# Kernel optimization log

Hardware: AMD Instinct MI355X
Metric: run time of the kernel (lower is better)

Reference implementation:

```python
import jax, jax.numpy as jnp
import numpy as np

B, T, C, H = 4, 2048, 768, 12
D = C // H  # head dim = 64


def setup_inputs() -> dict:
    key = jax.random.key(0)
    ks = jax.random.split(key, 4)
    scale = 0.02
    return {
        "x": jax.random.normal(ks[0], (B, T, C), dtype=jnp.float32),
        "W_attn": jax.random.normal(ks[1], (C, 3 * C), dtype=jnp.float32) * scale,
        "b_attn": jnp.zeros((3 * C,), dtype=jnp.float32),
        "W_proj": jax.random.normal(ks[2], (C, C), dtype=jnp.float32) * scale,
        "b_proj": jnp.zeros((C,), dtype=jnp.float32),
    }


def reference(x, W_attn, b_attn, W_proj, b_proj):
    Bsz, Tlen, Cdim = x.shape
    qkv = x @ W_attn + b_attn                    # [B,T,3C]
    q, k, v = jnp.split(qkv, 3, axis=-1)          # each [B,T,C]
    # [B,T,C] -> [B,H,T,D]
    def heads(t):
        return t.reshape(Bsz, Tlen, H, D).transpose(0, 2, 1, 3)
    q, k, v = heads(q), heads(k), heads(v)
    att = jnp.einsum("bhqd,bhkd->bhqk", q, k) * (1.0 / np.sqrt(D))
    # causal mask: position q attends to k <= q
    mask = jnp.tril(jnp.ones((Tlen, Tlen), dtype=bool))
    att = jnp.where(mask[None, None], att, -jnp.inf)
    att = jax.nn.softmax(att, axis=-1)
    y = jnp.einsum("bhqk,bhkd->bhqd", att, v)     # [B,H,T,D]
    y = y.transpose(0, 2, 1, 3).reshape(Bsz, Tlen, Cdim)
    return y @ W_proj + b_proj
```

## Files before the change

kernel.cpp:

```cpp
#include <hip/hip_runtime.h>

#define B_SZ   4
#define T_LEN  2048
#define C_DIM  768
#define H_NUM  12
#define THREEC (3 * C_DIM)
#define M_ROWS (B_SZ * T_LEN)
#define CAST_N8 (M_ROWS * C_DIM / 8)
#define CAST_BLOCKS (CAST_N8 / 256)
#define TP_BX ((THREEC + C_DIM) / 32)
#define TP_BY (C_DIM / 32)

typedef _Float16 f16;
typedef _Float16 half8 __attribute__((ext_vector_type(8)));
typedef _Float16 half4 __attribute__((ext_vector_type(4)));
typedef __fp16   pk2   __attribute__((ext_vector_type(2)));
typedef float    f32x4 __attribute__((ext_vector_type(4)));

#define GLD16(gaddr, laddr)                                                         \
  __builtin_amdgcn_global_load_lds(                                                 \
      (const __attribute__((address_space(1))) unsigned int*)(gaddr),               \
      (__attribute__((address_space(3))) unsigned int*)(laddr), 16, 0, 0)
#define MFMA16(a, b, c) __builtin_amdgcn_mfma_f32_16x16x32_f16(a, b, c, 0, 0, 0)

__global__ __launch_bounds__(256) void prep_kernel(
    const float* __restrict__ x, f16* __restrict__ xh,
    const float* __restrict__ Wa, const float* __restrict__ Wp,
    f16* __restrict__ WtA, f16* __restrict__ WtP) {
  __shared__ f16 tile[32][33];
  const int bid = blockIdx.x;
  if (bid < CAST_BLOCKS) {
    int i = bid * 256 + threadIdx.x;
    const float* s = x + (size_t)i * 8;
    half8 h;
#pragma unroll
    for (int u = 0; u < 8; ++u) h[u] = (f16)s[u];
    *(half8*)(xh + (size_t)i * 8) = h;
    return;
  }
  const int t = bid - CAST_BLOCKS;
  int bx = t % TP_BX;
  const int by = t / TP_BX;
  const float* W; f16* Wt; int N;
  if (bx < THREEC / 32) { W = Wa; Wt = WtA; N = THREEC; }
  else { W = Wp; Wt = WtP; N = C_DIM; bx -= THREEC / 32; }
  const int n0 = bx * 32, k0 = by * 32;
  const int tx = threadIdx.x & 31, ty = threadIdx.x >> 5;
#pragma unroll
  for (int i = 0; i < 4; ++i)
    tile[ty + i * 8][tx] = (f16)W[(size_t)(k0 + ty + i * 8) * N + n0 + tx];
  __syncthreads();
#pragma unroll
  for (int i = 0; i < 4; ++i)
    Wt[(size_t)(n0 + ty + i * 8) * C_DIM + k0 + tx] = tile[tx][ty + i * 8];
}

template <int BM, int BN, int OUT_F16, int SWZ>
__global__ __launch_bounds__(256) void gemm_f16_kernel(
    const f16* __restrict__ A, const f16* __restrict__ Bt,
    const float* __restrict__ bias, f16* __restrict__ OutH,
    float* __restrict__ OutF, int M, int N, int K) {
  __shared__ f16 As[BM * 64];
  __shared__ f16 Bs[BN * 64];
  const int tid = threadIdx.x;
  const int lane = tid & 63, wave = tid >> 6;
  const int lm = lane & 15, kq = lane >> 4, lm7 = lm & 7;
  constexpr int MT = BM / 32, NT = BN / 32;
  const int wm = (wave & 1) * (BM / 2), wn = (wave >> 1) * (BN / 2);

  int bx = blockIdx.x, by = blockIdx.y;
  if (SWZ) {
    const int nx = gridDim.x;
    const int lin = by * nx + bx;
    const int cpx = (nx * gridDim.y) >> 3;
    const int swz = (lin & 7) * cpx + (lin >> 3);
    bx = swz % nx;
    by = swz / nx;
  }
  const int row0 = by * BM, col0 = bx * BN;

  f32x4 acc[MT][NT] = {};

  for (int k0 = 0; k0 < K; k0 += 64) {
    __syncthreads();
#pragma unroll
    for (int i = 0; i < BM / 32; ++i) {
      int c = tid + i * 256;
      int r = c >> 3, cc = (c & 7) ^ (r & 7);
      GLD16(&A[(size_t)(row0 + r) * K + k0 + cc * 8],
            &As[(i * 256 + wave * 64) * 8]);
    }
#pragma unroll
    for (int i = 0; i < BN / 32; ++i) {
      int c = tid + i * 256;
      int r = c >> 3, cc = (c & 7) ^ (r & 7);
      GLD16(&Bt[(size_t)(col0 + r) * K + k0 + cc * 8],
            &Bs[(i * 256 + wave * 64) * 8]);
    }
    __syncthreads();
#pragma unroll
    for (int ks = 0; ks < 2; ++ks) {
      const int pos = (ks * 4 + kq);
      half8 af[MT], bf[NT];
#pragma unroll
      for (int t = 0; t < MT; ++t)
        af[t] = *(const half8*)&As[(wm + t * 16 + lm) * 64 + (pos ^ lm7) * 8];
#pragma unroll
      for (int t = 0; t < NT; ++t)
        bf[t] = *(const half8*)&Bs[(wn + t * 16 + lm) * 64 + (pos ^ lm7) * 8];
#pragma unroll
      for (int mt = 0; mt < MT; ++mt)
#pragma unroll
        for (int nt = 0; nt < NT; ++nt)
          acc[mt][nt] = MFMA16(af[mt], bf[nt], acc[mt][nt]);
    }
  }

#pragma unroll
  for (int mt = 0; mt < MT; ++mt) {
    const int row = row0 + wm + mt * 16 + kq * 4;
#pragma unroll
    for (int nt = 0; nt < NT; ++nt) {
      const int col = col0 + wn + nt * 16 + lm;
      const float bv = bias[col];
#pragma unroll
      for (int r = 0; r < 4; ++r) {
        float v = acc[mt][nt][r] + bv;
        if (OUT_F16)
          OutH[(size_t)(row + r) * N + col] = (f16)v;
        else
          OutF[(size_t)(row + r) * N + col] = v;
      }
    }
  }
}

__global__ __launch_bounds__(256) void v_transpose_kernel(
    const f16* __restrict__ qkv, f16* __restrict__ vt) {
  __shared__ f16 tile[64 * 68];
  const int bh = blockIdx.x, b = bh / H_NUM, h = bh % H_NUM;
  const int t0 = blockIdx.y * 64;
  const int tid = threadIdx.x;
#pragma unroll
  for (int i = 0; i < 2; ++i) {
    int c = tid + i * 256;
    int tr = c >> 3, doff = (c & 7) * 8;
    int pcol = ((tr >> 5) << 5) | (((tr >> 2) & 3) << 3) |
               (((tr >> 4) & 1) << 2) | (tr & 3);
    half8 v = *(const half8*)&qkv[(size_t)(b * T_LEN + t0 + tr) * THREEC + 2 * C_DIM + h * 64 + doff];
#pragma unroll
    for (int u = 0; u < 8; ++u) tile[(doff + u) * 68 + pcol] = v[u];
  }
  __syncthreads();
#pragma unroll
  for (int i = 0; i < 2; ++i) {
    int c = tid + i * 256;
    int d = c >> 3, toff = (c & 7) * 8;
    half8 v;
#pragma unroll
    for (int u = 0; u < 8; ++u) v[u] = tile[d * 68 + toff + u];
    *(half8*)&vt[((size_t)bh * 64 + d) * T_LEN + t0 + toff] = v;
  }
}

__global__ __launch_bounds__(256, 3) void attn_kernel(
    const f16* __restrict__ qkv, const f16* __restrict__ vt,
    f16* __restrict__ y) {
  __shared__ f16 Kt[3][64 * 64];
  __shared__ f16 Vt[3][64 * 64];

  const int bh = blockIdx.x, b = bh / H_NUM, h = bh % H_NUM;
  const int yb = blockIdx.y;
  const int qb = 15 - yb;
  const int tid = threadIdx.x, lane = tid & 63, wave = tid >> 6;
  const int lm = lane & 15, kq = lane >> 4, lm7 = lm & 7;
  const int cw = qb * 2 + (wave >> 1);
  const int qw = qb * 128 + wave * 32;
  const f16 qscale = (f16)(0.125f * 1.44269504f);

  half8 vones;
#pragma unroll
  for (int u = 0; u < 8; ++u) vones[u] = (f16)1.f;

  half8 bq[2][2];
#pragma unroll
  for (int cq = 0; cq < 2; ++cq)
#pragma unroll
    for (int c2 = 0; c2 < 2; ++c2) {
      half8 v = *(const half8*)&qkv[(size_t)(b * T_LEN + qw + cq * 16 + lm) * THREEC +
                                    h * 64 + c2 * 32 + kq * 8];
      bq[cq][c2] = v * qscale;
    }

  f32x4 o[4][2] = {};
  f32x4 ol[2] = {};

  f32x4 fz = {};
  asm volatile("" : "+v"(fz));

  const int srow = tid >> 3;
  const int scol = ((tid & 7) ^ (srow & 7)) * 8;
  const f16* kp = &qkv[(size_t)(b * T_LEN + srow) * THREEC + C_DIM + h * 64 + scol];
  const f16* vp = &vt[((size_t)bh * 64 + srow) * T_LEN + scol];
  const size_t kp2 = (size_t)32 * THREEC;
  const size_t vp2 = (size_t)32 * T_LEN;

  const int sbase = wave * 512;

  const int n_tiles = qb * 2 + 2;

  GLD16(kp, &Kt[0][sbase]);
  GLD16(kp + kp2, &Kt[0][2048 + sbase]);
  GLD16(vp, &Vt[0][sbase]);
  GLD16(vp + vp2, &Vt[0][2048 + sbase]);
  kp += (size_t)64 * THREEC;
  vp += 64;
  GLD16(kp, &Kt[1][sbase]);
  GLD16(kp + kp2, &Kt[1][2048 + sbase]);
  GLD16(vp, &Vt[1][sbase]);
  GLD16(vp + vp2, &Vt[1][2048 + sbase]);
  kp += (size_t)64 * THREEC;
  vp += 64;

  int cur = 0;
  for (int it = 0; it < n_tiles; ++it) {
    if (it + 2 < n_tiles) {
      const int pb = (cur == 0) ? 2 : cur - 1;
      GLD16(kp, &Kt[pb][sbase]);
      GLD16(kp + kp2, &Kt[pb][2048 + sbase]);
      GLD16(vp, &Vt[pb][sbase]);
      GLD16(vp + vp2, &Vt[pb][2048 + sbase]);
      kp += (size_t)64 * THREEC;
      vp += 64;
      asm volatile("s_waitcnt vmcnt(8)" ::: "memory");
    } else if (it + 1 < n_tiles) {
      asm volatile("s_waitcnt vmcnt(4)" ::: "memory");
    } else {
      asm volatile("s_waitcnt vmcnt(0)" ::: "memory");
    }
    __builtin_amdgcn_s_barrier();

    if (it <= cw) {
      __builtin_amdgcn_s_setprio(1);
      f32x4 s4[4][2];
#pragma unroll
      for (int ct = 0; ct < 4; ++ct) {
        const f16* kr = &Kt[cur][(ct * 16 + lm) * 64];
        half8 ak0 = *(const half8*)&kr[(kq ^ lm7) * 8];
        half8 ak1 = *(const half8*)&kr[((4 + kq) ^ lm7) * 8];
#pragma unroll
        for (int cq = 0; cq < 2; ++cq) {
          f32x4 z = MFMA16(ak0, bq[cq][0], fz);
          s4[ct][cq] = MFMA16(ak1, bq[cq][1], z);
        }
      }
      if (it == cw) {
        const int j0 = it * 64;
#pragma unroll
        for (int ct = 0; ct < 4; ++ct)
#pragma unroll
          for (int cq = 0; cq < 2; ++cq) {
            const int qrow = qw + cq * 16 + lm;
#pragma unroll
            for (int r = 0; r < 4; ++r)
              if (j0 + ct * 16 + kq * 4 + r > qrow) s4[ct][cq][r] = -1e30f;
          }
      }
      union { half8 h8; pk2 p2[4]; } pa0[2], pa1[2];
#pragma unroll
      for (int cq = 0; cq < 2; ++cq) {
        pa0[cq].p2[0] = __builtin_amdgcn_cvt_pkrtz(
            __builtin_amdgcn_exp2f(s4[0][cq][0]), __builtin_amdgcn_exp2f(s4[0][cq][1]));
        pa0[cq].p2[1] = __builtin_amdgcn_cvt_pkrtz(
            __builtin_amdgcn_exp2f(s4[0][cq][2]), __builtin_amdgcn_exp2f(s4[0][cq][3]));
        pa0[cq].p2[2] = __builtin_amdgcn_cvt_pkrtz(
            __builtin_amdgcn_exp2f(s4[1][cq][0]), __builtin_amdgcn_exp2f(s4[1][cq][1]));
        pa0[cq].p2[3] = __builtin_amdgcn_cvt_pkrtz(
            __builtin_amdgcn_exp2f(s4[1][cq][2]), __builtin_amdgcn_exp2f(s4[1][cq][3]));
        pa1[cq].p2[0] = __builtin_amdgcn_cvt_pkrtz(
            __builtin_amdgcn_exp2f(s4[2][cq][0]), __builtin_amdgcn_exp2f(s4[2][cq][1]));
        pa1[cq].p2[1] = __builtin_amdgcn_cvt_pkrtz(
            __builtin_amdgcn_exp2f(s4[2][cq][2]), __builtin_amdgcn_exp2f(s4[2][cq][3]));
        pa1[cq].p2[2] = __builtin_amdgcn_cvt_pkrtz(
            __builtin_amdgcn_exp2f(s4[3][cq][0]), __builtin_amdgcn_exp2f(s4[3][cq][1]));
        pa1[cq].p2[3] = __builtin_amdgcn_cvt_pkrtz(
            __builtin_amdgcn_exp2f(s4[3][cq][2]), __builtin_amdgcn_exp2f(s4[3][cq][3]));
      }

#pragma unroll
      for (int dt = 0; dt < 4; ++dt) {
        const f16* vr = &Vt[cur][(dt * 16 + lm) * 64];
        half8 bv0 = *(const half8*)&vr[(kq ^ lm7) * 8];
        half8 bv1 = *(const half8*)&vr[((4 + kq) ^ lm7) * 8];
#pragma unroll
        for (int cq = 0; cq < 2; ++cq) {
          o[dt][cq] = MFMA16(pa0[cq].h8, bv0, o[dt][cq]);
          o[dt][cq] = MFMA16(pa1[cq].h8, bv1, o[dt][cq]);
        }
      }
#pragma unroll
      for (int cq = 0; cq < 2; ++cq) {
        ol[cq] = MFMA16(pa0[cq].h8, vones, ol[cq]);
        ol[cq] = MFMA16(pa1[cq].h8, vones, ol[cq]);
      }
      __builtin_amdgcn_s_setprio(0);
    }

    __builtin_amdgcn_s_barrier();
    cur = (cur == 2) ? 0 : cur + 1;
  }

#pragma unroll
  for (int cq = 0; cq < 2; ++cq)
#pragma unroll
    for (int r = 0; r < 4; ++r) {
      const float inv = 1.f / ol[cq][r];
      const size_t base =
          (size_t)(b * T_LEN + qw + cq * 16 + kq * 4 + r) * C_DIM + h * 64;
#pragma unroll
      for (int dt = 0; dt < 4; ++dt)
        y[base + dt * 16 + lm] = (f16)(o[dt][cq][r] * inv);
    }
}

extern "C" void kernel_launch(void* const* d_in, const int* in_sizes, int n_in,
                              void* d_out, int out_size, void* d_ws, size_t ws_size,
                              hipStream_t stream) {
  const float* x      = (const float*)d_in[0];
  const float* W_attn = (const float*)d_in[1];
  const float* b_attn = (const float*)d_in[2];
  const float* W_proj = (const float*)d_in[3];
  const float* b_proj = (const float*)d_in[4];
  float* out = (float*)d_out;

  const int M = M_ROWS;
  auto align256 = [](size_t v) { return (v + 255) & ~(size_t)255; };
  char* ws = (char*)d_ws;
  f16* xh   = (f16*)ws; ws += align256((size_t)M * C_DIM * 2);
  f16* WtA  = (f16*)ws; ws += align256((size_t)THREEC * C_DIM * 2);
  f16* WtP  = (f16*)ws; ws += align256((size_t)C_DIM * C_DIM * 2);
  f16* qkvh = (f16*)ws; ws += align256((size_t)M * THREEC * 2);
  f16* vtg  = (f16*)ws; ws += align256((size_t)B_SZ * H_NUM * 64 * T_LEN * 2);
  f16* yh   = (f16*)ws; ws += align256((size_t)M * C_DIM * 2);

  prep_kernel<<<CAST_BLOCKS + TP_BX * TP_BY, 256, 0, stream>>>(
      x, xh, W_attn, W_proj, WtA, WtP);

  gemm_f16_kernel<128, 128, 1, 1><<<dim3(THREEC / 128, M / 128), 256, 0, stream>>>(
      xh, WtA, b_attn, qkvh, nullptr, M, THREEC, C_DIM);

  v_transpose_kernel<<<dim3(B_SZ * H_NUM, T_LEN / 64), 256, 0, stream>>>(qkvh, vtg);

  attn_kernel<<<dim3(B_SZ * H_NUM, 16), 256, 0, stream>>>(qkvh, vtg, yh);

  gemm_f16_kernel<128, 64, 0, 1><<<dim3(C_DIM / 64, M / 128), 256, 0, stream>>>(
      yh, WtP, b_proj, nullptr, out, M, C_DIM, C_DIM);
}
```

Baseline: 184.6 us.

## Double attention query tile per block to 256 rows, 64 per wave

Each attention block now covers 256 query rows instead of 128, and each wave handles 64 rows (4 MFMA row groups) instead of 32. The grid's y dimension halves, so every K/V tile staged in LDS is reused by twice as many queries, cutting global K/V traffic and barrier overhead per query. The QK^T, mask and exp work is restructured to run one row group at a time to keep register pressure in check. In exchange, register use grows (launch bounds drop to 2 blocks per CU), there are half as many blocks to balance the causal triangle, and waves within a block sit idle more often on the diagonal tiles.

```diff
diff --git a/kernel.cpp b/kernel.cpp
--- a/kernel.cpp
+++ b/kernel.cpp
@@ -163,28 +163,27 @@
   }
 }
 
-__global__ __launch_bounds__(256, 3) void attn_kernel(
+__global__ __launch_bounds__(256, 2) void attn_kernel(
     const f16* __restrict__ qkv, const f16* __restrict__ vt,
     f16* __restrict__ y) {
   __shared__ f16 Kt[3][64 * 64];
   __shared__ f16 Vt[3][64 * 64];
 
   const int bh = blockIdx.x, b = bh / H_NUM, h = bh % H_NUM;
-  const int yb = blockIdx.y;
-  const int qb = 15 - yb;
+  const int qb = 7 - blockIdx.y;
   const int tid = threadIdx.x, lane = tid & 63, wave = tid >> 6;
   const int lm = lane & 15, kq = lane >> 4, lm7 = lm & 7;
-  const int cw = qb * 2 + (wave >> 1);
-  const int qw = qb * 128 + wave * 32;
+  const int cw = qb * 4 + wave;
+  const int qw = qb * 256 + wave * 64;
   const f16 qscale = (f16)(0.125f * 1.44269504f);
 
   half8 vones;
 #pragma unroll
   for (int u = 0; u < 8; ++u) vones[u] = (f16)1.f;
 
-  half8 bq[2][2];
-#pragma unroll
-  for (int cq = 0; cq < 2; ++cq)
+  half8 bq[4][2];
+#pragma unroll
+  for (int cq = 0; cq < 4; ++cq)
 #pragma unroll
     for (int c2 = 0; c2 < 2; ++c2) {
       half8 v = *(const half8*)&qkv[(size_t)(b * T_LEN + qw + cq * 16 + lm) * THREEC +
@@ -192,8 +191,8 @@
       bq[cq][c2] = v * qscale;
     }
 
-  f32x4 o[4][2] = {};
-  f32x4 ol[2] = {};
+  f32x4 o[4][4] = {};
+  f32x4 ol[4] = {};
 
   f32x4 fz = {};
   asm volatile("" : "+v"(fz));
@@ -207,7 +206,7 @@
 
   const int sbase = wave * 512;
 
-  const int n_tiles = qb * 2 + 2;
+  const int n_tiles = qb * 4 + 4;
 
   GLD16(kp, &Kt[0][sbase]);
   GLD16(kp + kp2, &Kt[0][2048 + sbase]);
@@ -242,49 +241,49 @@
 
     if (it <= cw) {
       __builtin_amdgcn_s_setprio(1);
-      f32x4 s4[4][2];
+      half8 ak[4][2];
 #pragma unroll
       for (int ct = 0; ct < 4; ++ct) {
         const f16* kr = &Kt[cur][(ct * 16 + lm) * 64];
-        half8 ak0 = *(const half8*)&kr[(kq ^ lm7) * 8];
-        half8 ak1 = *(const half8*)&kr[((4 + kq) ^ lm7) * 8];
-#pragma unroll
-        for (int cq = 0; cq < 2; ++cq) {
-          f32x4 z = MFMA16(ak0, bq[cq][0], fz);
-          s4[ct][cq] = MFMA16(ak1, bq[cq][1], z);
+        ak[ct][0] = *(const half8*)&kr[(kq ^ lm7) * 8];
+        ak[ct][1] = *(const half8*)&kr[((4 + kq) ^ lm7) * 8];
+      }
+      union { half8 h8; pk2 p2[4]; } pa0[4], pa1[4];
+      const int j0 = it * 64;
+#pragma unroll
+      for (int cq = 0; cq < 4; ++cq) {
+        f32x4 s4[4];
+#pragma unroll
+        for (int ct = 0; ct < 4; ++ct) {
+          f32x4 z = MFMA16(ak[ct][0], bq[cq][0], fz);
+          s4[ct] = MFMA16(ak[ct][1], bq[cq][1], z);
         }
-      }
-      if (it == cw) {
-        const int j0 = it * 64;
-#pragma unroll
-        for (int ct = 0; ct < 4; ++ct)
-#pragma unroll
-          for (int cq = 0; cq < 2; ++cq) {
-            const int qrow = qw + cq * 16 + lm;
+        if (it == cw) {
+          const int qrow = qw + cq * 16 + lm;
+#pragma unroll
+          for (int ct = 0; ct < 4; ++ct)
 #pragma unroll
             for (int r = 0; r < 4; ++r)
-              if (j0 + ct * 16 + kq * 4 + r > qrow) s4[ct][cq][r] = -1e30f;
-          }
-      }
-      union { half8 h8; pk2 p2[4]; } pa0[2], pa1[2];
-#pragma unroll
-      for (int cq = 0; cq < 2; ++cq) {
+              if (j0 + ct * 16 + kq * 4 + r > qrow) s4[ct][r] = -1e30f;
+        }
         pa0[cq].p2[0] = __builtin_amdgcn_cvt_pkrtz(
-            __builtin_amdgcn_exp2f(s4[0][cq][0]), __builtin_amdgcn_exp2f(s4[0][cq][1]));
+            __builtin_amdgcn_exp2f(s4[0][0]), __builtin_amdgcn_exp2f(s4[0][1]));
         pa0[cq].p2[1] = __builtin_amdgcn_cvt_pkrtz(
-            __builtin_amdgcn_exp2f(s4[0][cq][2]), __builtin_amdgcn_exp2f(s4[0][cq][3]));
+            __builtin_amdgcn_exp2f(s4[0][2]), __builtin_amdgcn_exp2f(s4[0][3]));
         pa0[cq].p2[2] = __builtin_amdgcn_cvt_pkrtz(
-            __builtin_amdgcn_exp2f(s4[1][cq][0]), __builtin_amdgcn_exp2f(s4[1][cq][1]));
+            __builtin_amdgcn_exp2f(s4[1][0]), __builtin_amdgcn_exp2f(s4[1][1]));
         pa0[cq].p2[3] = __builtin_amdgcn_cvt_pkrtz(
-            __builtin_amdgcn_exp2f(s4[1][cq][2]), __builtin_amdgcn_exp2f(s4[1][cq][3]));
+            __builtin_amdgcn_exp2f(s4[1][2]), __builtin_amdgcn_exp2f(s4[1][3]));
         pa1[cq].p2[0] = __builtin_amdgcn_cvt_pkrtz(
-            __builtin_amdgcn_exp2f(s4[2][cq][0]), __builtin_amdgcn_exp2f(s4[2][cq][1]));
+            __builtin_amdgcn_exp2f(s4[2][0]), __builtin_amdgcn_exp2f(s4[2][1]));
         pa1[cq].p2[1] = __builtin_amdgcn_cvt_pkrtz(
-            __builtin_amdgcn_exp2f(s4[2][cq][2]), __builtin_amdgcn_exp2f(s4[2][cq][3]));
+            __builtin_amdgcn_exp2f(s4[2][2]), __builtin_amdgcn_exp2f(s4[2][3]));
         pa1[cq].p2[2] = __builtin_amdgcn_cvt_pkrtz(
-            __builtin_amdgcn_exp2f(s4[3][cq][0]), __builtin_amdgcn_exp2f(s4[3][cq][1]));
+            __builtin_amdgcn_exp2f(s4[3][0]), __builtin_amdgcn_exp2f(s4[3][1]));
         pa1[cq].p2[3] = __builtin_amdgcn_cvt_pkrtz(
-            __builtin_amdgcn_exp2f(s4[3][cq][2]), __builtin_amdgcn_exp2f(s4[3][cq][3]));
+            __builtin_amdgcn_exp2f(s4[3][2]), __builtin_amdgcn_exp2f(s4[3][3]));
+        ol[cq] = MFMA16(pa0[cq].h8, vones, ol[cq]);
+        ol[cq] = MFMA16(pa1[cq].h8, vones, ol[cq]);
       }
 
 #pragma unroll
@@ -293,16 +292,11 @@
         half8 bv0 = *(const half8*)&vr[(kq ^ lm7) * 8];
         half8 bv1 = *(const half8*)&vr[((4 + kq) ^ lm7) * 8];
 #pragma unroll
-        for (int cq = 0; cq < 2; ++cq) {
+        for (int cq = 0; cq < 4; ++cq) {
           o[dt][cq] = MFMA16(pa0[cq].h8, bv0, o[dt][cq]);
           o[dt][cq] = MFMA16(pa1[cq].h8, bv1, o[dt][cq]);
         }
       }
-#pragma unroll
-      for (int cq = 0; cq < 2; ++cq) {
-        ol[cq] = MFMA16(pa0[cq].h8, vones, ol[cq]);
-        ol[cq] = MFMA16(pa1[cq].h8, vones, ol[cq]);
-      }
       __builtin_amdgcn_s_setprio(0);
     }
 
@@ -311,7 +305,7 @@
   }
 
 #pragma unroll
-  for (int cq = 0; cq < 2; ++cq)
+  for (int cq = 0; cq < 4; ++cq)
 #pragma unroll
     for (int r = 0; r < 4; ++r) {
       const float inv = 1.f / ol[cq][r];
@@ -351,7 +345,7 @@
 
   v_transpose_kernel<<<dim3(B_SZ * H_NUM, T_LEN / 64), 256, 0, stream>>>(qkvh, vtg);
 
-  attn_kernel<<<dim3(B_SZ * H_NUM, 16), 256, 0, stream>>>(qkvh, vtg, yh);
+  attn_kernel<<<dim3(B_SZ * H_NUM, 8), 256, 0, stream>>>(qkvh, vtg, yh);
 
   gemm_f16_kernel<128, 64, 0, 1><<<dim3(C_DIM / 64, M / 128), 256, 0, stream>>>(
       yh, WtP, b_proj, nullptr, out, M, C_DIM, C_DIM);
```

After: 200.7 us. 8.7% more time.
